# Optimization experiments

Measured on AMD Instinct MI355X. Metric: run time of the kernel, lower is better.

Reference implementation:

```python
import jax, jax.numpy as jnp
from jax import lax
import numpy as np

DN = ('NDHWC', 'DHWIO', 'NDHWC')

def _conv(x, W):
    # stride-1 kernel-3 sparse conv on dense grid: SAME conv; absent voxels are zero
    return lax.conv_general_dilated(x, W, (1, 1, 1), 'SAME', dimension_numbers=DN)

def _tconv(x, W):
    # kernel-2 stride-2 generative transpose conv: exactly doubles each spatial dim
    return lax.conv_transpose(x, W, (2, 2, 2), 'VALID', dimension_numbers=DN)

def _pool(h):
    B, D1, D2, D3, C = h.shape
    return h.reshape(B, D1 // 2, 2, D2 // 2, 2, D3 // 2, 2, C).max(axis=(2, 4, 6))

def _pool_mask(m):
    B, D1, D2, D3 = m.shape
    return m.reshape(B, D1 // 2, 2, D2 // 2, 2, D3 // 2, 2).max(axis=(2, 4, 6))

def _up_mask(m):
    return jnp.repeat(jnp.repeat(jnp.repeat(m, 2, axis=1), 2, axis=2), 2, axis=3)

def setup_inputs() -> dict:
    key = jax.random.key(0)
    ks = jax.random.split(key, 6)
    B, G = 2, 128
    x = jax.random.normal(ks[0], (B, G, G, G, 1), dtype=jnp.float32)
    occ = jax.random.randint(ks[1], (B, G, G, G), 0, 10, dtype=jnp.int32)
    def xavier(k, shape):
        fan_in = np.prod(shape[:-1]); fan_out = shape[-1]
        std = np.sqrt(2.0 / (fan_in + fan_out)).astype(np.float32)
        return jax.random.normal(k, shape, dtype=jnp.float32) * std
    W1 = xavier(ks[2], (3, 3, 3, 1, 16))
    W2 = xavier(ks[3], (3, 3, 3, 16, 4))
    Wt1 = xavier(ks[4], (2, 2, 2, 4, 16))
    Wt2 = xavier(ks[5], (2, 2, 2, 16, 1))
    return {"x": x, "W1": W1, "W2": W2, "Wt1": Wt1, "Wt2": Wt2, "occ": occ}

def reference(x, W1, W2, Wt1, Wt2, occ):
    m0 = (occ == 0).astype(x.dtype)            # occupancy mask at full res
    xm = x * m0[..., None]
    h = jax.nn.relu(_conv(xm, W1)) * m0[..., None]   # coords unchanged
    h = _pool(h); m1 = _pool_mask(m0)                # stride-2 max pool on sparse coords
    h = jax.nn.relu(_conv(h, W2)) * m1[..., None]
    h = _pool(h); m2 = _pool_mask(m1)
    m3 = _up_mask(m2)                                # transpose conv emits all children coords
    h = jax.nn.relu(_tconv(h, Wt1)) * m3[..., None]
    m4 = _up_mask(m3)
    out = jax.nn.sigmoid(_tconv(h, Wt2)) * m4[..., None]
    return out
```

## Files before the change

### kernel.cpp

```cpp
#include <hip/hip_runtime.h>
#include <hip/hip_fp16.h>

#define G 128

typedef _Float16 h2_t __attribute__((ext_vector_type(2)));

union U16 { uint4 u; h2_t h2[4]; };
union HV  { uint4 u; h2_t h2[4]; };

__device__ __forceinline__ float dot2f(h2_t a, h2_t b, float c) {
#if __has_builtin(__builtin_amdgcn_fdot2)
    return __builtin_amdgcn_fdot2(a, b, c, false);
#else
    return c + (float)a.x * (float)b.x + (float)a.y * (float)b.y;
#endif
}

__device__ __forceinline__ h2_t h2max(h2_t a, h2_t b) {
#if __has_builtin(__builtin_elementwise_max)
    return __builtin_elementwise_max(a, b);
#else
    h2_t r;
    r.x = a.x > b.x ? a.x : b.x;
    r.y = a.y > b.y ? a.y : b.y;
    return r;
#endif
}

__device__ __forceinline__ float dot4(float4 a, float4 b) {
    return a.x * b.x + a.y * b.y + a.z * b.z + a.w * b.w;
}

__global__ void k_prep(const float* __restrict__ W1, const float* __restrict__ W2,
                       __half* __restrict__ w1h, __half* __restrict__ w2h)
{
    int i = blockIdx.x * 256 + threadIdx.x;
    if (i < 216) {
        int tap = i >> 3, p = i & 7;
        w1h[2 * i]     = __float2half(W1[tap * 16 + 2 * p]);
        w1h[2 * i + 1] = __float2half(W1[tap * 16 + 2 * p + 1]);
    }
    if (i < 864) {
        int t = i >> 5, r = i & 31, co = r >> 3, p = r & 7;
        w2h[2 * i]     = __float2half(W2[t * 64 + (2 * p) * 4 + co]);
        w2h[2 * i + 1] = __float2half(W2[t * 64 + (2 * p + 1) * 4 + co]);
    }
}

__global__ __launch_bounds__(256, 2)
void k_conv1_pool(const float* __restrict__ x, const int* __restrict__ occ,
                  const h2_t* __restrict__ w1h,
                  __half* __restrict__ h1p, float* __restrict__ m1)
{
    __shared__ _Float16      sx[10 * 18 * 18];
    __shared__ unsigned char sm[10 * 18 * 18];

    const int bx = blockIdx.x, by = blockIdx.y;
    const int b  = blockIdx.z >> 4, zt = blockIdx.z & 15;
    const int tid = threadIdx.x;

    const int z0 = zt * 8 - 1, y0 = by * 16 - 1, x0 = bx * 16 - 1;
    const int base_b = b * G * G * G;

    #pragma unroll
    for (int r = 0; r < 13; ++r) {
        int i = r * 256 + tid;
        if (i < 3240) {
            int lz = i / 324, rr = i - lz * 324;
            int ly = rr / 18, lx = rr - ly * 18;
            int gz = z0 + lz, gy = y0 + ly, gx = x0 + lx;
            bool inb = (unsigned)gz < 128u && (unsigned)gy < 128u &&
                       (unsigned)gx < 128u;
            int oc = 1; float xv = 0.f;
            if (inb) {
                int gi = base_b + (gz * G + gy) * G + gx;
                oc = occ[gi];
                xv = x[gi];
            }
            bool mm = inb && (oc == 0);
            sx[i] = mm ? (_Float16)xv : (_Float16)0.f;
            sm[i] = mm ? 1 : 0;
        }
    }
    __syncthreads();

    const int tx = tid & 7, ty = (tid >> 3) & 7, tz = tid >> 6;

    const h2_t zero = (h2_t)(_Float16)0.f;
    h2_t best[8];
    #pragma unroll
    for (int c = 0; c < 8; ++c) best[c] = zero;
    int anym = 0;

    #pragma unroll
    for (int pos = 0; pos < 8; ++pos) {
        const int dz = pos >> 2, dy = (pos >> 1) & 1, dx = pos & 1;
        const int cz = 2 * tz + dz, cy = 2 * ty + dy, cx = 2 * tx + dx;
        const int cb = (cz + 1) * 324 + (cy + 1) * 18 + (cx + 1);
        if (sm[cb]) {
            anym = 1;
            h2_t acc[8];
            #pragma unroll
            for (int c = 0; c < 8; ++c) acc[c] = zero;
            #pragma unroll
            for (int kz = 0; kz < 3; ++kz)
            #pragma unroll
            for (int ky = 0; ky < 3; ++ky)
            #pragma unroll
            for (int kx = 0; kx < 3; ++kx) {
                _Float16 v = sx[cb + (kz - 1) * 324 + (ky - 1) * 18 + (kx - 1)];
                h2_t v2 = {v, v};
                const h2_t* w = &w1h[((kz * 3 + ky) * 3 + kx) * 8];
                #pragma unroll
                for (int c = 0; c < 8; ++c) acc[c] = v2 * w[c] + acc[c];
            }
            #pragma unroll
            for (int c = 0; c < 8; ++c) best[c] = h2max(best[c], h2max(acc[c], zero));
        }
    }

    const int pz = zt * 4 + tz, py = by * 8 + ty, px = bx * 8 + tx;
    const int vidx = ((b * 64 + pz) * 64 + py) * 64 + px;
    HV p0, p1;
    #pragma unroll
    for (int c = 0; c < 4; ++c) { p0.h2[c] = best[c]; p1.h2[c] = best[4 + c]; }
    uint4* o = (uint4*)&h1p[(size_t)vidx * 16];
    o[0] = p0.u;
    o[1] = p1.u;
    m1[vidx] = anym ? 1.f : 0.f;
}

__global__ __launch_bounds__(256)
void k_conv2_dec(const __half* __restrict__ h1p, const float* __restrict__ m1,
                 const h2_t* __restrict__ w2h,
                 const float* __restrict__ Wt1, const float* __restrict__ Wt2,
                 float* __restrict__ out)
{
    __shared__ uint4  tile[1100];
    __shared__ float4 wt1[128];
    __shared__ float4 wt2[32];
    __shared__ float4 sh_h[64];
    __shared__ float  sh_m[64];

    const int bx = blockIdx.x, by = blockIdx.y;
    const int b  = blockIdx.z >> 3, bz = blockIdx.z & 7;
    const int tid = threadIdx.x;

    if (tid < 128) wt1[tid] = ((const float4*)Wt1)[tid];
    if (tid < 32)  wt2[tid] = ((const float4*)Wt2)[tid];

    const int z0 = bz * 8 - 1, y0 = by * 8 - 1, x0 = bx * 8 - 1;

    const int dy = tid & 1, dz = (tid >> 1) & 1;
    const int qx = (tid >> 2) & 3, Y = (tid >> 4) & 3, Z = (tid >> 6) & 3;
    const int cx0 = 2 * qx, cy = 2 * Y + dy, cz = 2 * Z + dz;

    float acc[2][4] = {{0.f, 0.f, 0.f, 0.f}, {0.f, 0.f, 0.f, 0.f}};

    for (int h = 0; h < 2; ++h) {
        if (h) __syncthreads();
        #pragma unroll
        for (int it = 0; it < 5; ++it) {
            int g = it * 256 + tid;
            if (g < 1100) {
                int z = g / 110, r = g - z * 110, y = r / 11, xx = r - y * 11;
                int gz = z0 + z, gy = y0 + y, gx = x0 + xx;
                uint4 a = make_uint4(0u, 0u, 0u, 0u);
                if ((unsigned)gz < 64u && (unsigned)gy < 64u && (unsigned)gx < 64u)
                    a = ((const uint4*)&h1p[(size_t)(((b * 64 + gz) * 64 + gy) * 64 + gx) * 16])[h];
                tile[g] = a;
            }
        }
        __syncthreads();

        #pragma unroll
        for (int kz = 0; kz < 3; ++kz)
        #pragma unroll
        for (int ky = 0; ky < 3; ++ky) {
            const int rb = (cz + kz) * 110 + (cy + ky) * 11 + cx0;
            h2_t hp[4][4];
            #pragma unroll
            for (int xi = 0; xi < 4; ++xi) {
                U16 a; a.u = tile[rb + xi];
                #pragma unroll
                for (int p = 0; p < 4; ++p) hp[xi][p] = a.h2[p];
            }
            const int t3 = (kz * 3 + ky) * 3;
            #pragma unroll
            for (int kx = 0; kx < 3; ++kx) {
                const h2_t* w = w2h + (t3 + kx) * 32 + 4 * h;
                #pragma unroll
                for (int j = 0; j < 2; ++j) {
                    #pragma unroll
                    for (int co = 0; co < 4; ++co) {
                        float a = acc[j][co];
                        #pragma unroll
                        for (int p = 0; p < 4; ++p)
                            a = dot2f(hp[kx + j][p], w[co * 8 + p], a);
                        acc[j][co] = a;
                    }
                }
            }
        }
    }

    const int gcz = bz * 8 + cz, gcy = by * 8 + cy, gcx = bx * 8 + cx0;
    const float mv0 = m1[((b * 64 + gcz) * 64 + gcy) * 64 + gcx];
    const float mv1 = m1[((b * 64 + gcz) * 64 + gcy) * 64 + gcx + 1];
    float m = fmaxf(mv0, mv1);
    float r0 = fmaxf(fmaxf(acc[0][0], 0.f) * mv0, fmaxf(acc[1][0], 0.f) * mv1);
    float r1 = fmaxf(fmaxf(acc[0][1], 0.f) * mv0, fmaxf(acc[1][1], 0.f) * mv1);
    float r2 = fmaxf(fmaxf(acc[0][2], 0.f) * mv0, fmaxf(acc[1][2], 0.f) * mv1);
    float r3 = fmaxf(fmaxf(acc[0][3], 0.f) * mv0, fmaxf(acc[1][3], 0.f) * mv1);

    #pragma unroll
    for (int mask = 1; mask <= 2; mask <<= 1) {
        r0 = fmaxf(r0, __shfl_xor(r0, mask));
        r1 = fmaxf(r1, __shfl_xor(r1, mask));
        r2 = fmaxf(r2, __shfl_xor(r2, mask));
        r3 = fmaxf(r3, __shfl_xor(r3, mask));
        m  = fmaxf(m,  __shfl_xor(m,  mask));
    }
    if ((tid & 3) == 0) {
        int p = Z * 16 + Y * 4 + qx;
        sh_h[p] = make_float4(r0, r1, r2, r3);
        sh_m[p] = m;
    }
    __syncthreads();

    {
        const int p  = tid >> 2;
        const int a  = (tid >> 1) & 1;
        const int bb = tid & 1;
        const int pZ = p >> 4, pY = (p >> 2) & 3, pq = p & 3;
        const int pz = bz * 4 + pZ, py = by * 4 + pY, pxq = bx * 4 + pq;

        const float mm = sh_m[p];
        const float4 hv = sh_h[p];

        const int b0q = ((((1 - a) * 2 + (1 - bb)) * 2) + 1) * 16;
        const int b1q = ((((1 - a) * 2 + (1 - bb)) * 2) + 0) * 16;
        float4 t0q[4], t1q[4];
        #pragma unroll
        for (int q = 0; q < 4; ++q) {
            float4 a0 = wt1[b0q + q],      a1 = wt1[b0q + 4 + q];
            float4 a2 = wt1[b0q + 8 + q],  a3 = wt1[b0q + 12 + q];
            float4 c0 = wt1[b1q + q],      c1 = wt1[b1q + 4 + q];
            float4 c2 = wt1[b1q + 8 + q],  c3 = wt1[b1q + 12 + q];
            float4 s0, s1;
            s0.x = hv.x * a0.x + hv.y * a1.x + hv.z * a2.x + hv.w * a3.x;
            s0.y = hv.x * a0.y + hv.y * a1.y + hv.z * a2.y + hv.w * a3.y;
            s0.z = hv.x * a0.z + hv.y * a1.z + hv.z * a2.z + hv.w * a3.z;
            s0.w = hv.x * a0.w + hv.y * a1.w + hv.z * a2.w + hv.w * a3.w;
            s1.x = hv.x * c0.x + hv.y * c1.x + hv.z * c2.x + hv.w * c3.x;
            s1.y = hv.x * c0.y + hv.y * c1.y + hv.z * c2.y + hv.w * c3.y;
            s1.z = hv.x * c0.z + hv.y * c1.z + hv.z * c2.z + hv.w * c3.z;
            s1.w = hv.x * c0.w + hv.y * c1.w + hv.z * c2.w + hv.w * c3.w;
            t0q[q] = make_float4(fmaxf(s0.x, 0.f), fmaxf(s0.y, 0.f),
                                 fmaxf(s0.z, 0.f), fmaxf(s0.w, 0.f));
            t1q[q] = make_float4(fmaxf(s1.x, 0.f), fmaxf(s1.y, 0.f),
                                 fmaxf(s1.z, 0.f), fmaxf(s1.w, 0.f));
        }

        #pragma unroll
        for (int e = 0; e < 2; ++e) {
            #pragma unroll
            for (int f = 0; f < 2; ++f) {
                const int d  = 4 * pz + 2 * a + e;
                const int hh = 4 * py + 2 * bb + f;
                const int be = ((1 - e) * 2 + (1 - f)) * 2;
                const float4* wg0 = &wt2[(be + 1) * 4];
                const float4* wg1 = &wt2[(be + 0) * 4];
                float s00 = dot4(t0q[0], wg0[0]) + dot4(t0q[1], wg0[1])
                          + dot4(t0q[2], wg0[2]) + dot4(t0q[3], wg0[3]);
                float s01 = dot4(t0q[0], wg1[0]) + dot4(t0q[1], wg1[1])
                          + dot4(t0q[2], wg1[2]) + dot4(t0q[3], wg1[3]);
                float s10 = dot4(t1q[0], wg0[0]) + dot4(t1q[1], wg0[1])
                          + dot4(t1q[2], wg0[2]) + dot4(t1q[3], wg0[3]);
                float s11 = dot4(t1q[0], wg1[0]) + dot4(t1q[1], wg1[1])
                          + dot4(t1q[2], wg1[2]) + dot4(t1q[3], wg1[3]);
                float4 o;
                o.x = mm / (1.f + __expf(-s00));
                o.y = mm / (1.f + __expf(-s01));
                o.z = mm / (1.f + __expf(-s10));
                o.w = mm / (1.f + __expf(-s11));
                *(float4*)&out[((b * G + d) * G + hh) * G + 4 * pxq] = o;
            }
        }
    }
}

extern "C" void kernel_launch(void* const* d_in, const int* in_sizes, int n_in,
                              void* d_out, int out_size, void* d_ws, size_t ws_size,
                              hipStream_t stream) {
    (void)in_sizes; (void)n_in; (void)out_size; (void)ws_size;
    const float* x   = (const float*)d_in[0];
    const float* W1  = (const float*)d_in[1];
    const float* W2  = (const float*)d_in[2];
    const float* Wt1 = (const float*)d_in[3];
    const float* Wt2 = (const float*)d_in[4];
    const int*   occ = (const int*)d_in[5];
    float* out = (float*)d_out;

    char* ws = (char*)d_ws;
    __half* h1p = (__half*)ws;
    float*  m1  = (float*)(ws + 8388608ull * sizeof(__half));
    __half* w2h = (__half*)(m1 + 524288);
    __half* w1h = w2h + 1728;

    k_prep<<<dim3(4), dim3(256), 0, stream>>>(W1, W2, w1h, w2h);
    k_conv1_pool<<<dim3(8, 8, 32), dim3(256), 0, stream>>>(x, occ, (const h2_t*)w1h, h1p, m1);
    k_conv2_dec<<<dim3(8, 8, 16), dim3(256), 0, stream>>>(h1p, m1, (const h2_t*)w2h, Wt1, Wt2, out);
}
```

Measured before the change: 166.8 us.

## Compact active voxels in conv1 and pool via LDS atomicMax

```diff
diff --git a/kernel.cpp b/kernel.cpp
--- a/kernel.cpp
+++ b/kernel.cpp
@@ -47,58 +47,94 @@
     }
 }
 
-__global__ __launch_bounds__(256, 2)
+__global__ __launch_bounds__(256, 4)
 void k_conv1_pool(const float* __restrict__ x, const int* __restrict__ occ,
                   const h2_t* __restrict__ w1h,
                   __half* __restrict__ h1p, float* __restrict__ m1)
 {
-    __shared__ _Float16      sx[10 * 18 * 18];
-    __shared__ unsigned char sm[10 * 18 * 18];
+    __shared__ __align__(16) _Float16      sx[10 * 18 * 24];
+    __shared__ __align__(4)  unsigned char smB[10 * 18 * 24];
+    __shared__ __align__(16) int           pacc[16 * 256];
+    __shared__ unsigned short              slist[2048];
+    __shared__ int                         scnt;
 
     const int bx = blockIdx.x, by = blockIdx.y;
     const int b  = blockIdx.z >> 4, zt = blockIdx.z & 15;
     const int tid = threadIdx.x;
 
-    const int z0 = zt * 8 - 1, y0 = by * 16 - 1, x0 = bx * 16 - 1;
+    const int z0 = zt * 8 - 1, y0 = by * 16 - 1;
     const int base_b = b * G * G * G;
 
+    if (tid == 0) scnt = 0;
+
+    {
+        uint4 z4 = make_uint4(0u, 0u, 0u, 0u);
+        uint4* p4 = (uint4*)pacc;
+        p4[tid] = z4; p4[tid + 256] = z4; p4[tid + 512] = z4; p4[tid + 768] = z4;
+    }
+
     #pragma unroll
-    for (int r = 0; r < 13; ++r) {
-        int i = r * 256 + tid;
-        if (i < 3240) {
-            int lz = i / 324, rr = i - lz * 324;
-            int ly = rr / 18, lx = rr - ly * 18;
-            int gz = z0 + lz, gy = y0 + ly, gx = x0 + lx;
-            bool inb = (unsigned)gz < 128u && (unsigned)gy < 128u &&
-                       (unsigned)gx < 128u;
-            int oc = 1; float xv = 0.f;
-            if (inb) {
-                int gi = base_b + (gz * G + gy) * G + gx;
-                oc = occ[gi];
-                xv = x[gi];
-            }
-            bool mm = inb && (oc == 0);
-            sx[i] = mm ? (_Float16)xv : (_Float16)0.f;
-            sm[i] = mm ? 1 : 0;
+    for (int it = 0; it < 5; ++it) {
+        int c = it * 256 + tid;
+        if (c < 1080) {
+            int row = c / 6, seg = c - row * 6;
+            int lz  = row / 18, ly = row - lz * 18;
+            int gz = z0 + lz, gy = y0 + ly;
+            int gxc = (bx << 4) - 4 + (seg << 2);
+            int4   o4 = make_int4(1, 1, 1, 1);
+            float4 x4 = make_float4(0.f, 0.f, 0.f, 0.f);
+            if ((unsigned)gz < 128u && (unsigned)gy < 128u && (unsigned)gxc < 128u) {
+                const int gi = base_b + (gz * G + gy) * G + gxc;
+                o4 = *(const int4*)(occ + gi);
+                x4 = *(const float4*)(x + gi);
+            }
+            unsigned mbits = (o4.x == 0 ? 0x1u : 0u) | (o4.y == 0 ? 0x100u : 0u)
+                           | (o4.z == 0 ? 0x10000u : 0u) | (o4.w == 0 ? 0x1000000u : 0u);
+            h2_t p01, p23;
+            p01.x = (o4.x == 0) ? (_Float16)x4.x : (_Float16)0.f;
+            p01.y = (o4.y == 0) ? (_Float16)x4.y : (_Float16)0.f;
+            p23.x = (o4.z == 0) ? (_Float16)x4.z : (_Float16)0.f;
+            p23.y = (o4.w == 0) ? (_Float16)x4.w : (_Float16)0.f;
+            const int eo = row * 24 + (seg << 2);
+            union { uint2 u; h2_t h[2]; } pk;
+            pk.h[0] = p01; pk.h[1] = p23;
+            *(uint2*)&sx[eo] = pk.u;
+            *(unsigned*)&smB[eo] = mbits;
         }
     }
     __syncthreads();
 
     const int tx = tid & 7, ty = (tid >> 3) & 7, tz = tid >> 6;
-
-    const h2_t zero = (h2_t)(_Float16)0.f;
-    h2_t best[8];
-    #pragma unroll
-    for (int c = 0; c < 8; ++c) best[c] = zero;
+    const int lane = tid & 63;
     int anym = 0;
 
     #pragma unroll
     for (int pos = 0; pos < 8; ++pos) {
         const int dz = pos >> 2, dy = (pos >> 1) & 1, dx = pos & 1;
         const int cz = 2 * tz + dz, cy = 2 * ty + dy, cx = 2 * tx + dx;
-        const int cb = (cz + 1) * 324 + (cy + 1) * 18 + (cx + 1);
-        if (sm[cb]) {
-            anym = 1;
+        const int act = smB[((cz + 1) * 18 + (cy + 1)) * 24 + cx + 4];
+        anym |= act;
+        unsigned long long bal = __ballot(act != 0);
+        int wtot = __popcll(bal);
+        int wbase = 0;
+        if (lane == 0 && wtot) wbase = atomicAdd(&scnt, wtot);
+        wbase = __shfl(wbase, 0);
+        if (act) {
+            int pre = __popcll(bal & ((1ull << lane) - 1ull));
+            slist[wbase + pre] = (unsigned short)((cz << 8) | (cy << 4) | cx);
+        }
+    }
+    __syncthreads();
+
+    const int n = scnt;
+
+    const h2_t zero = (h2_t)(_Float16)0.f;
+    for (int kb = 0; kb < n; kb += 256) {
+        const int idx = kb + tid;
+        if (idx < n) {
+            const int code = slist[idx];
+            const int cz = code >> 8, cy = (code >> 4) & 15, cx = code & 15;
+            const int sb = ((cz + 1) * 18 + (cy + 1)) * 24 + cx + 4;
             h2_t acc[8];
             #pragma unroll
             for (int c = 0; c < 8; ++c) acc[c] = zero;
@@ -108,22 +144,36 @@
             for (int ky = 0; ky < 3; ++ky)
             #pragma unroll
             for (int kx = 0; kx < 3; ++kx) {
-                _Float16 v = sx[cb + (kz - 1) * 324 + (ky - 1) * 18 + (kx - 1)];
+                _Float16 v = sx[sb + (kz - 1) * 432 + (ky - 1) * 24 + (kx - 1)];
                 h2_t v2 = {v, v};
                 const h2_t* w = &w1h[((kz * 3 + ky) * 3 + kx) * 8];
                 #pragma unroll
                 for (int c = 0; c < 8; ++c) acc[c] = v2 * w[c] + acc[c];
             }
-            #pragma unroll
-            for (int c = 0; c < 8; ++c) best[c] = h2max(best[c], h2max(acc[c], zero));
-        }
-    }
+            const int cell = (cz >> 1) * 64 + (cy >> 1) * 8 + (cx >> 1);
+            #pragma unroll
+            for (int c = 0; c < 8; ++c) {
+                float fa = fmaxf((float)acc[c].x, 0.f);
+                float fb = fmaxf((float)acc[c].y, 0.f);
+                atomicMax(&pacc[(2 * c) * 256 + cell],     __float_as_int(fa));
+                atomicMax(&pacc[(2 * c + 1) * 256 + cell], __float_as_int(fb));
+            }
+        }
+    }
+    __syncthreads();
 
     const int pz = zt * 4 + tz, py = by * 8 + ty, px = bx * 8 + tx;
     const int vidx = ((b * 64 + pz) * 64 + py) * 64 + px;
     HV p0, p1;
     #pragma unroll
-    for (int c = 0; c < 4; ++c) { p0.h2[c] = best[c]; p1.h2[c] = best[4 + c]; }
+    for (int c = 0; c < 4; ++c) {
+        h2_t a, bq;
+        a.x  = (_Float16)__int_as_float(pacc[(2 * c) * 256 + tid]);
+        a.y  = (_Float16)__int_as_float(pacc[(2 * c + 1) * 256 + tid]);
+        bq.x = (_Float16)__int_as_float(pacc[(8 + 2 * c) * 256 + tid]);
+        bq.y = (_Float16)__int_as_float(pacc[(9 + 2 * c) * 256 + tid]);
+        p0.h2[c] = a; p1.h2[c] = bq;
+    }
     uint4* o = (uint4*)&h1p[(size_t)vidx * 16];
     o[0] = p0.u;
     o[1] = p1.u;
```

Result: faster. 144.0 us (-13.6%).
